# Kernel tuning notes

Measured on AMD Instinct MI355X. Metric: run time of the kernel, lower is better.

## Reference

```python
import jax, jax.numpy as jnp
import numpy as np

N_NODES = 50000
N_EDGES = 800000
IN_DIM = 128
HID = 128
NUM_CLASSES = 2


def setup_inputs() -> dict:
    key = jax.random.key(0)
    ks = jax.random.split(key, 16)
    inp = {
        "adj_row": jax.random.randint(ks[0], (N_EDGES,), 0, N_NODES),
        "adj_col": jax.random.randint(ks[1], (N_EDGES,), 0, N_NODES),
        "adj_vals": jax.random.uniform(ks[2], (N_EDGES,), dtype=jnp.float32),
        "input_feature": jax.random.normal(ks[3], (N_NODES, IN_DIM), dtype=jnp.float32),
        "graph_indicator": jax.random.randint(ks[4], (N_NODES,), 0, 64),
        # GCN layer params (kaiming-uniform-ish init; zeros bias like the torch module)
        "W1": jax.random.uniform(ks[5], (IN_DIM, HID), jnp.float32, -1, 1) * np.sqrt(6.0 / IN_DIM),
        "b1": jnp.zeros((HID,), jnp.float32),
        "W2": jax.random.uniform(ks[6], (HID, HID), jnp.float32, -1, 1) * np.sqrt(6.0 / HID),
        "b2": jnp.zeros((HID,), jnp.float32),
        "W3": jax.random.uniform(ks[7], (HID, HID), jnp.float32, -1, 1) * np.sqrt(6.0 / HID),
        "b3": jnp.zeros((HID,), jnp.float32),
        # fc params (torch.nn.Linear default init range)
        "fcW1": jax.random.uniform(ks[8], (3 * HID, HID), jnp.float32, -1, 1) / np.sqrt(3 * HID),
        "fcb1": jax.random.uniform(ks[9], (HID,), jnp.float32, -1, 1) / np.sqrt(3 * HID),
        "fcW2": jax.random.uniform(ks[10], (HID, HID // 2), jnp.float32, -1, 1) / np.sqrt(HID),
        "fcb2": jax.random.uniform(ks[11], (HID // 2,), jnp.float32, -1, 1) / np.sqrt(HID),
        "fcW3": jax.random.uniform(ks[12], (HID // 2, NUM_CLASSES), jnp.float32, -1, 1) / np.sqrt(HID // 2),
        "fcb3": jax.random.uniform(ks[13], (NUM_CLASSES,), jnp.float32, -1, 1) / np.sqrt(HID // 2),
    }
    return inp


def _gcn_layer(row, col, vals, x, W, b, n_nodes):
    # support = X @ W  -> dense GEMM
    support = x @ W
    # sparse.mm(A, support): out[i] = sum_{e: row[e]=i} vals[e] * support[col[e]]
    msgs = support[col] * vals[:, None]  # [E, D] gather + scale
    agg = jax.ops.segment_sum(msgs, row, num_segments=n_nodes)
    return agg + b


def reference(adj_row, adj_col, adj_vals, input_feature, graph_indicator,
              W1, b1, W2, b2, W3, b3, fcW1, fcb1, fcW2, fcb2, fcW3, fcb3):
    n = input_feature.shape[0]
    g1 = jax.nn.relu(_gcn_layer(adj_row, adj_col, adj_vals, input_feature, W1, b1, n))
    g2 = jax.nn.relu(_gcn_layer(adj_row, adj_col, adj_vals, g1, W2, b2, n))
    g3 = jax.nn.relu(_gcn_layer(adj_row, adj_col, adj_vals, g2, W3, b3, n))
    feat = jnp.concatenate([g1, g2, g3], axis=1)  # [N, 3*HID]
    h = jax.nn.relu(feat @ fcW1 + fcb1)
    h = jax.nn.relu(h @ fcW2 + fcb2)
    logits = h @ fcW3 + fcb3
    return logits
```

## Files before the change

### kernel.cpp

```cpp
#include <hip/hip_runtime.h>
#include <hip/hip_bf16.h>

#define N_NODES 50000
#define N_EDGES 800000
#define NBK 391
#define BCAP 2560

static inline int cdiv(int a, int b) { return (a + b - 1) / b; }

typedef __attribute__((ext_vector_type(8))) short short8;
typedef __attribute__((ext_vector_type(4))) float f32x4;

__device__ __forceinline__ float b2f(unsigned short u) {
    union { unsigned int i; float f; } c;
    c.i = ((unsigned int)u) << 16;
    return c.f;
}
__device__ __forceinline__ unsigned short f2bb(float f) {
    __hip_bfloat16 h = __float2bfloat16(f);
    return *(unsigned short*)&h;
}

__device__ __forceinline__ void pack_one(const float* __restrict__ W,
                                         __hip_bfloat16* __restrict__ out,
                                         int K, int N, int t) {
    int lane = t & 63;
    int kc = (t >> 6) % (K / 32);
    int nt = (t >> 6) / (K / 32);
    int kbase = kc * 32 + (lane >> 4) * 8;
    int col = nt * 16 + (lane & 15);
    __hip_bfloat16* dst = out + (size_t)t * 8;
#pragma unroll
    for (int j = 0; j < 8; ++j)
        dst[j] = __float2bfloat16(W[(size_t)(kbase + j) * N + col]);
}

__global__ __launch_bounds__(256)
void stage1_kernel(const int* __restrict__ row, const int* __restrict__ col,
                   const float* __restrict__ vals, int* __restrict__ bcursor,
                   int2* __restrict__ tmp, int E,
                   const float* __restrict__ x, __hip_bfloat16* __restrict__ support,
                   int M,
                   const float* __restrict__ W1, const float* __restrict__ W2,
                   const float* __restrict__ W3, const float* __restrict__ fcW1,
                   const float* __restrict__ fcW2,
                   __hip_bfloat16* __restrict__ pW2, __hip_bfloat16* __restrict__ pW3,
                   __hip_bfloat16* __restrict__ pfcW1, __hip_bfloat16* __restrict__ pfcW2) {
    __shared__ unsigned short As[64][136];
    __shared__ int hist[NBK];
    __shared__ int base[NBK];
    const int b = blockIdx.x;
    const int tid = threadIdx.x;

    if (b < 196) {
        const int CH = 4096;
        int e0 = b * CH;
        for (int i = tid; i < NBK; i += 256) hist[i] = 0;
        __syncthreads();
        for (int i = tid; i < CH; i += 256) {
            int e = e0 + i;
            if (e < E) atomicAdd(&hist[row[e] >> 7], 1);
        }
        __syncthreads();
        for (int i = tid; i < NBK; i += 256) {
            int c = hist[i];
            base[i] = (c > 0) ? (i * BCAP + atomicAdd(&bcursor[i], c)) : 0;
            hist[i] = 0;
        }
        __syncthreads();
        for (int i = tid; i < CH; i += 256) {
            int e = e0 + i;
            if (e < E) {
                int r = row[e];
                int bk = r >> 7;
                int rk = atomicAdd(&hist[bk], 1);
                tmp[base[bk] + rk] = make_int2(((r & 127) << 16) | col[e],
                                               __float_as_int(vals[e]));
            }
        }
        return;
    }

    if (b < 978) {
        const int wave = tid >> 6;
        const int lane = tid & 63;
        const int ln15 = lane & 15;
        const int quad = lane >> 4;
        const int m0 = (b - 196) * 64;

        short8 bfr[4][2];
#pragma unroll
        for (int kc = 0; kc < 4; ++kc)
#pragma unroll
            for (int h = 0; h < 2; ++h)
#pragma unroll
                for (int j = 0; j < 8; ++j)
                    bfr[kc][h][j] = (short)f2bb(
                        W1[(size_t)(kc * 32 + quad * 8 + j) * 128 + (wave * 2 + h) * 16 + ln15]);

#pragma unroll
        for (int i = 0; i < 4; ++i) {
            int idx = tid + i * 256;
            int r = idx >> 4;
            int c8 = (idx & 15) * 8;
            uint4 pk = {0, 0, 0, 0};
            if (m0 + r < M) {
                const float* src = &x[(size_t)(m0 + r) * 128 + c8];
                float4 a = *(const float4*)src;
                float4 bq = *(const float4*)(src + 4);
                pk.x = f2bb(a.x) | ((unsigned int)f2bb(a.y) << 16);
                pk.y = f2bb(a.z) | ((unsigned int)f2bb(a.w) << 16);
                pk.z = f2bb(bq.x) | ((unsigned int)f2bb(bq.y) << 16);
                pk.w = f2bb(bq.z) | ((unsigned int)f2bb(bq.w) << 16);
            }
            *(uint4*)&As[r][c8] = pk;
        }
        __syncthreads();

        f32x4 acc[4][2];
#pragma unroll
        for (int s = 0; s < 4; ++s)
#pragma unroll
            for (int h = 0; h < 2; ++h) acc[s][h] = (f32x4){0.f, 0.f, 0.f, 0.f};
#pragma unroll
        for (int kc = 0; kc < 4; ++kc) {
            short8 af[4];
#pragma unroll
            for (int s = 0; s < 4; ++s)
                af[s] = *(const short8*)&As[s * 16 + ln15][kc * 32 + quad * 8];
#pragma unroll
            for (int s = 0; s < 4; ++s)
#pragma unroll
                for (int h = 0; h < 2; ++h)
                    acc[s][h] = __builtin_amdgcn_mfma_f32_16x16x32_bf16(
                        af[s], bfr[kc][h], acc[s][h], 0, 0, 0);
        }
#pragma unroll
        for (int s = 0; s < 4; ++s)
#pragma unroll
            for (int h = 0; h < 2; ++h) {
                int cl = (wave * 2 + h) * 16 + ln15;
#pragma unroll
                for (int r = 0; r < 4; ++r) {
                    int rw = m0 + s * 16 + quad * 4 + r;
                    if (rw < M)
                        support[(size_t)rw * 128 + cl] = __float2bfloat16(acc[s][h][r]);
                }
            }
        return;
    }

    int pb = b - 978;
    if (pb < 8)       pack_one(W2,  pW2,  128, 128, pb * 256 + tid);
    else if (pb < 16) pack_one(W3,  pW3,  128, 128, (pb - 8) * 256 + tid);
    else if (pb < 40) pack_one(fcW1, pfcW1, 384, 128, (pb - 16) * 256 + tid);
    else              pack_one(fcW2, pfcW2, 128, 64, (pb - 40) * 256 + tid);
}


__global__ __launch_bounds__(512)
void bscan_kernel(const int* __restrict__ bcursor, int* __restrict__ bbase) {
    __shared__ int s[512];
    int t = threadIdx.x;
    int v = (t < NBK) ? bcursor[t] : 0;
    s[t] = v;
    __syncthreads();
    for (int off = 1; off < 512; off <<= 1) {
        int u = (t >= off) ? s[t - off] : 0;
        __syncthreads();
        s[t] += u;
        __syncthreads();
    }
    if (t < NBK) bbase[t] = s[t] - v;
    if (t == NBK - 1) bbase[NBK] = s[t];
}

__global__ __launch_bounds__(256)
void binB_kernel(const int2* __restrict__ tmp, const int* __restrict__ bcursor,
                 const int* __restrict__ bbase, int* __restrict__ row_ptr,
                 int2* __restrict__ epack, int N) {
    int b = blockIdx.x;
    int r0 = b << 7;
    int nr = N - r0; if (nr > 128) nr = 128;
    __shared__ int cnt[128];
    __shared__ int cur[128];
    int t = threadIdx.x;
    if (t < 128) cnt[t] = 0;
    __syncthreads();
    int slab = b * BCAP;
    int send = slab + bcursor[b];
    int obase = bbase[b];
    for (int i = slab + t; i < send; i += 256)
        atomicAdd(&cnt[tmp[i].x >> 16], 1);
    __syncthreads();
    if (t < 128) cur[t] = cnt[t];
    __syncthreads();
    for (int off = 1; off < 128; off <<= 1) {
        int u = (t >= off && t < 128) ? cur[t - off] : 0;
        __syncthreads();
        if (t < 128) cur[t] += u;
        __syncthreads();
    }
    if (t < 128) {
        int ex = cur[t] - cnt[t];
        int pos = obase + ex;
        cur[t] = pos;
        if (t < nr) row_ptr[r0 + t] = pos;
    }
    if (b == NBK - 1 && t == 128) row_ptr[N] = bbase[NBK];
    __syncthreads();
    for (int i = slab + t; i < send; i += 256) {
        int2 v = tmp[i];
        int rl = v.x >> 16;
        int c = v.x & 0xffff;
        int pos = atomicAdd(&cur[rl], 1);
        epack[pos] = make_int2(c, v.y);
    }
}

__global__ __launch_bounds__(256, 3)
void mfma_gemm(const __hip_bfloat16* __restrict__ A, int lda,
               const __hip_bfloat16* __restrict__ pW,
               __hip_bfloat16* __restrict__ C, int M) {
    __shared__ unsigned short As[64][136];
    const int tid = threadIdx.x;
    const int wave = tid >> 6;
    const int lane = tid & 63;
    const int ln15 = lane & 15;
    const int quad = lane >> 4;
    const int m0 = blockIdx.x * 64;
    const int ntw = wave * 2;

    f32x4 acc[4][2];
#pragma unroll
    for (int s = 0; s < 4; ++s)
#pragma unroll
        for (int h = 0; h < 2; ++h) acc[s][h] = (f32x4){0.f, 0.f, 0.f, 0.f};

#pragma unroll
    for (int i = 0; i < 4; ++i) {
        int idx = tid + i * 256;
        int r = idx >> 4;
        int c8 = (idx & 15) * 8;
        uint4 v = *(const uint4*)&A[(size_t)(m0 + r) * lda + c8];
        *(uint4*)&As[r][c8] = v;
    }
    __syncthreads();
#pragma unroll
    for (int kc = 0; kc < 4; ++kc) {
        short8 af[4];
#pragma unroll
        for (int s = 0; s < 4; ++s)
            af[s] = *(const short8*)&As[s * 16 + ln15][kc * 32 + quad * 8];
        short8 bf[2];
#pragma unroll
        for (int h = 0; h < 2; ++h)
            bf[h] = *(const short8*)&pW[((size_t)((ntw + h) * 4 + kc) * 64 + lane) * 8];
#pragma unroll
        for (int s = 0; s < 4; ++s)
#pragma unroll
            for (int h = 0; h < 2; ++h)
                acc[s][h] = __builtin_amdgcn_mfma_f32_16x16x32_bf16(
                    af[s], bf[h], acc[s][h], 0, 0, 0);
    }

#pragma unroll
    for (int s = 0; s < 4; ++s)
#pragma unroll
        for (int h = 0; h < 2; ++h) {
            int cl = (ntw + h) * 16 + ln15;
#pragma unroll
            for (int r = 0; r < 4; ++r) {
                int rw = m0 + s * 16 + quad * 4 + r;
                if (rw < M)
                    C[(size_t)rw * 128 + cl] = __float2bfloat16(acc[s][h][r]);
            }
        }
}

__global__ __launch_bounds__(256)
void spmm_kernel(const int* __restrict__ row_ptr, const int2* __restrict__ epack,
                 const __hip_bfloat16* __restrict__ support,
                 const float* __restrict__ bias, __hip_bfloat16* __restrict__ out,
                 int ldo, int n) {
    int wv = threadIdx.x >> 6;
    int l = threadIdx.x & 63;
    int node = blockIdx.x * 4 + wv;
    if (node >= n) return;
    const long long* ep = (const long long*)epack;
    int start = row_ptr[node], end = row_ptr[node + 1];
    float ax = 0.f, ay = 0.f;
    int p = start;
    for (; p + 8 <= end; p += 8) {
        long long v[8];
        ushort2 u[8];
#pragma unroll
        for (int j = 0; j < 8; ++j) v[j] = ep[p + j];
#pragma unroll
        for (int j = 0; j < 8; ++j)
            u[j] = *(const ushort2*)&support[(size_t)(unsigned int)(v[j] & 0xffffffff) * 128 + l * 2];
#pragma unroll
        for (int j = 0; j < 8; ++j) {
            float f = __int_as_float((int)(v[j] >> 32));
            ax += f * b2f(u[j].x);
            ay += f * b2f(u[j].y);
        }
    }
    for (; p < end; ++p) {
        long long v0 = ep[p];
        ushort2 u0 = *(const ushort2*)&support[(size_t)(unsigned int)(v0 & 0xffffffff) * 128 + l * 2];
        float f0 = __int_as_float((int)(v0 >> 32));
        ax += f0 * b2f(u0.x);
        ay += f0 * b2f(u0.y);
    }
    unsigned int packed = (unsigned int)f2bb(fmaxf(ax + bias[l * 2 + 0], 0.f))
                        | ((unsigned int)f2bb(fmaxf(ay + bias[l * 2 + 1], 0.f)) << 16);
    __builtin_nontemporal_store(packed, (unsigned int*)&out[(size_t)node * ldo + l * 2]);
}

__global__ __launch_bounds__(256, 3)
void fc123_kernel(const __hip_bfloat16* __restrict__ featb,
                  const __hip_bfloat16* __restrict__ pfcW1,
                  const float* __restrict__ fcb1,
                  const __hip_bfloat16* __restrict__ pfcW2,
                  const float* __restrict__ fcb2,
                  const float* __restrict__ fcW3, const float* __restrict__ fcb3,
                  float* __restrict__ out, int M) {
    __shared__ unsigned short As[64][136];
    __shared__ float w3s[128];
    __shared__ float b3s[2];
    const int tid = threadIdx.x;
    const int wave = tid >> 6;
    const int lane = tid & 63;
    const int ln15 = lane & 15;
    const int quad = lane >> 4;
    const int m0 = blockIdx.x * 64;
    if (tid < 128) w3s[tid] = fcW3[tid];
    if (tid < 2) b3s[tid] = fcb3[tid];

    f32x4 acc[4][2];
#pragma unroll
    for (int s = 0; s < 4; ++s)
#pragma unroll
        for (int h = 0; h < 2; ++h) acc[s][h] = (f32x4){0.f, 0.f, 0.f, 0.f};
    for (int kb = 0; kb < 3; ++kb) {
#pragma unroll
        for (int i = 0; i < 4; ++i) {
            int idx = tid + i * 256;
            int r = idx >> 4;
            int c8 = (idx & 15) * 8;
            uint4 v = *(const uint4*)&featb[(size_t)(m0 + r) * 384 + kb * 128 + c8];
            *(uint4*)&As[r][c8] = v;
        }
        __syncthreads();
#pragma unroll
        for (int kc = 0; kc < 4; ++kc) {
            short8 af[4];
#pragma unroll
            for (int s = 0; s < 4; ++s)
                af[s] = *(const short8*)&As[s * 16 + ln15][kc * 32 + quad * 8];
            short8 bf[2];
#pragma unroll
            for (int h = 0; h < 2; ++h) {
                int kcg = kb * 4 + kc;
                bf[h] = *(const short8*)&pfcW1[((size_t)((wave * 2 + h) * 12 + kcg) * 64 + lane) * 8];
            }
#pragma unroll
            for (int s = 0; s < 4; ++s)
#pragma unroll
                for (int h = 0; h < 2; ++h)
                    acc[s][h] = __builtin_amdgcn_mfma_f32_16x16x32_bf16(
                        af[s], bf[h], acc[s][h], 0, 0, 0);
        }
        __syncthreads();
    }
#pragma unroll
    for (int s = 0; s < 4; ++s)
#pragma unroll
        for (int h = 0; h < 2; ++h) {
            int col = (wave * 2 + h) * 16 + ln15;
            float bv = fcb1[col];
#pragma unroll
            for (int r = 0; r < 4; ++r) {
                int row = s * 16 + quad * 4 + r;
                As[row][col] = f2bb(fmaxf(acc[s][h][r] + bv, 0.f));
            }
        }
    __syncthreads();

    f32x4 acc2[4];
#pragma unroll
    for (int s = 0; s < 4; ++s) acc2[s] = (f32x4){0.f, 0.f, 0.f, 0.f};
#pragma unroll
    for (int kc = 0; kc < 4; ++kc) {
        short8 af[4];
#pragma unroll
        for (int s = 0; s < 4; ++s)
            af[s] = *(const short8*)&As[s * 16 + ln15][kc * 32 + quad * 8];
        short8 bfw = *(const short8*)&pfcW2[((size_t)(wave * 4 + kc) * 64 + lane) * 8];
#pragma unroll
        for (int s = 0; s < 4; ++s)
            acc2[s] = __builtin_amdgcn_mfma_f32_16x16x32_bf16(af[s], bfw, acc2[s], 0, 0, 0);
    }
    __syncthreads();
    {
        int col2 = wave * 16 + ln15;
        float bv = fcb2[col2];
#pragma unroll
        for (int s = 0; s < 4; ++s)
#pragma unroll
            for (int r = 0; r < 4; ++r) {
                int row = s * 16 + quad * 4 + r;
                As[row][col2] = f2bb(fmaxf(acc2[s][r] + bv, 0.f));
            }
    }
    __syncthreads();

    if (tid < 128) {
        int row = tid >> 1, cls = tid & 1;
        int grow = m0 + row;
        if (grow < M) {
            float a = b3s[cls];
#pragma unroll
            for (int k = 0; k < 64; ++k)
                a += b2f(As[row][k]) * w3s[k * 2 + cls];
            out[(size_t)grow * 2 + cls] = a;
        }
    }
}

extern "C" void kernel_launch(void* const* d_in, const int* in_sizes, int n_in,
                              void* d_out, int out_size, void* d_ws, size_t ws_size,
                              hipStream_t stream) {
    const int*   adj_row  = (const int*)d_in[0];
    const int*   adj_col  = (const int*)d_in[1];
    const float* adj_vals = (const float*)d_in[2];
    const float* x        = (const float*)d_in[3];
    const float* W1   = (const float*)d_in[5];
    const float* b1   = (const float*)d_in[6];
    const float* W2   = (const float*)d_in[7];
    const float* b2   = (const float*)d_in[8];
    const float* W3   = (const float*)d_in[9];
    const float* b3   = (const float*)d_in[10];
    const float* fcW1 = (const float*)d_in[11];
    const float* fcb1 = (const float*)d_in[12];
    const float* fcW2 = (const float*)d_in[13];
    const float* fcb2 = (const float*)d_in[14];
    const float* fcW3 = (const float*)d_in[15];
    const float* fcb3 = (const float*)d_in[16];
    float* out = (float*)d_out;

    const int N = N_NODES, E = N_EDGES;
    const int Mpad = 50048;

    char* p = (char*)d_ws;
    auto alloc = [&](size_t bytes) {
        char* q = p;
        p += (bytes + 255) & ~(size_t)255;
        return q;
    };
    __hip_bfloat16* featb    = (__hip_bfloat16*)alloc((size_t)Mpad * 384 * 2);
    __hip_bfloat16* supportb = (__hip_bfloat16*)alloc((size_t)Mpad * 128 * 2);
    __hip_bfloat16* pW2   = (__hip_bfloat16*)alloc(16384 * 2);
    __hip_bfloat16* pW3   = (__hip_bfloat16*)alloc(16384 * 2);
    __hip_bfloat16* pfcW1 = (__hip_bfloat16*)alloc(49152 * 2);
    __hip_bfloat16* pfcW2 = (__hip_bfloat16*)alloc(8192 * 2);
    int*   row_ptr   = (int*)alloc((size_t)(N + 1) * 4);
    int*   bbase     = (int*)alloc((size_t)(NBK + 1) * 4);
    int*   bcursor   = (int*)alloc((size_t)NBK * 4);
    int2*  epack     = (int2*)alloc((size_t)E * 8);
    int2*  tmp       = (int2*)alloc((size_t)NBK * BCAP * 8);

    hipMemsetAsync(bcursor, 0, (size_t)NBK * 4, stream);
    stage1_kernel<<<1022, 256, 0, stream>>>(adj_row, adj_col, adj_vals, bcursor, tmp, E,
                                            x, supportb, N,
                                            W1, W2, W3, fcW1, fcW2,
                                            pW2, pW3, pfcW1, pfcW2);
    bscan_kernel<<<1, 512, 0, stream>>>(bcursor, bbase);
    binB_kernel<<<NBK, 256, 0, stream>>>(tmp, bcursor, bbase, row_ptr, epack, N);

    const int gemmGrid = cdiv(N, 64);
    const int spmmGrid = cdiv(N, 4);

    spmm_kernel<<<spmmGrid, 256, 0, stream>>>(row_ptr, epack, supportb, b1,
                                              featb + 0, 384, N);
    mfma_gemm<<<gemmGrid, 256, 0, stream>>>(featb + 0, 384, pW2, supportb, N);
    spmm_kernel<<<spmmGrid, 256, 0, stream>>>(row_ptr, epack, supportb, b2,
                                              featb + 128, 384, N);
    mfma_gemm<<<gemmGrid, 256, 0, stream>>>(featb + 128, 384, pW3, supportb, N);
    spmm_kernel<<<spmmGrid, 256, 0, stream>>>(row_ptr, epack, supportb, b3,
                                              featb + 256, 384, N);

    fc123_kernel<<<gemmGrid, 256, 0, stream>>>(featb, pfcW1, fcb1, pfcW2, fcb2,
                                               fcW3, fcb3, out, N);
}
```

Measured before the change: 296.4 us.

## Pad CSR rows to multiples of eight and software-pipeline SpMM gathers

The binning kernel now pads each row's edge list to a multiple of eight with zero-weight entries pointing at node 0, and records per-row end pointers in a new row_end array. Each 128-row bucket gets its own slack region. This removes the scalar tail loop in the SpMM kernel. The SpMM loop is also double-buffered: it issues the next eight edge loads and support gathers before accumulating the previous batch, to hide gather latency. In exchange, padding adds extra gathers on average degree-16 rows and uses more registers per lane.

```diff
diff --git a/kernel.cpp b/kernel.cpp
--- a/kernel.cpp
+++ b/kernel.cpp
@@ -5,6 +5,7 @@
 #define N_EDGES 800000
 #define NBK 391
 #define BCAP 2560
+#define PADSLACK 896
 
 static inline int cdiv(int a, int b) { return (a + b - 1) / b; }
 
@@ -178,22 +179,24 @@
 __global__ __launch_bounds__(256)
 void binB_kernel(const int2* __restrict__ tmp, const int* __restrict__ bcursor,
                  const int* __restrict__ bbase, int* __restrict__ row_ptr,
-                 int2* __restrict__ epack, int N) {
+                 int* __restrict__ row_end, int2* __restrict__ epack, int N) {
     int b = blockIdx.x;
     int r0 = b << 7;
     int nr = N - r0; if (nr > 128) nr = 128;
     __shared__ int cnt[128];
     __shared__ int cur[128];
+    __shared__ int rpos[128];
     int t = threadIdx.x;
     if (t < 128) cnt[t] = 0;
     __syncthreads();
     int slab = b * BCAP;
     int send = slab + bcursor[b];
-    int obase = bbase[b];
     for (int i = slab + t; i < send; i += 256)
         atomicAdd(&cnt[tmp[i].x >> 16], 1);
     __syncthreads();
-    if (t < 128) cur[t] = cnt[t];
+    int rcnt = (t < 128) ? cnt[t] : 0;
+    int pc = (rcnt + 7) & ~7;
+    if (t < 128) cur[t] = pc;
     __syncthreads();
     for (int off = 1; off < 128; off <<= 1) {
         int u = (t >= off && t < 128) ? cur[t - off] : 0;
@@ -201,13 +204,16 @@
         if (t < 128) cur[t] += u;
         __syncthreads();
     }
+    int obase = bbase[b] + b * PADSLACK;
     if (t < 128) {
-        int ex = cur[t] - cnt[t];
-        int pos = obase + ex;
+        int pos = obase + cur[t] - pc;
+        rpos[t] = pos;
         cur[t] = pos;
-        if (t < nr) row_ptr[r0 + t] = pos;
-    }
-    if (b == NBK - 1 && t == 128) row_ptr[N] = bbase[NBK];
+        if (t < nr) {
+            row_ptr[r0 + t] = pos;
+            row_end[r0 + t] = pos + pc;
+        }
+    }
     __syncthreads();
     for (int i = slab + t; i < send; i += 256) {
         int2 v = tmp[i];
@@ -215,6 +221,12 @@
         int c = v.x & 0xffff;
         int pos = atomicAdd(&cur[rl], 1);
         epack[pos] = make_int2(c, v.y);
+    }
+    if (t < 128) {
+        int pos = rpos[t];
+#pragma unroll 1
+        for (int i = pos + rcnt; i < pos + pc; ++i)
+            epack[i] = make_int2(0, 0);
     }
 }
 
@@ -279,7 +291,8 @@
 }
 
 __global__ __launch_bounds__(256)
-void spmm_kernel(const int* __restrict__ row_ptr, const int2* __restrict__ epack,
+void spmm_kernel(const int* __restrict__ row_ptr, const int* __restrict__ row_end,
+                 const int2* __restrict__ epack,
                  const __hip_bfloat16* __restrict__ support,
                  const float* __restrict__ bias, __hip_bfloat16* __restrict__ out,
                  int ldo, int n) {
@@ -288,30 +301,45 @@
     int node = blockIdx.x * 4 + wv;
     if (node >= n) return;
     const long long* ep = (const long long*)epack;
-    int start = row_ptr[node], end = row_ptr[node + 1];
+    int p = row_ptr[node], end = row_end[node];
     float ax = 0.f, ay = 0.f;
-    int p = start;
-    for (; p + 8 <= end; p += 8) {
-        long long v[8];
-        ushort2 u[8];
+    long long v[8];
+    ushort2 u[8];
+    bool have = false;
+    if (p < end) {
 #pragma unroll
         for (int j = 0; j < 8; ++j) v[j] = ep[p + j];
 #pragma unroll
         for (int j = 0; j < 8; ++j)
-            u[j] = *(const ushort2*)&support[(size_t)(unsigned int)(v[j] & 0xffffffff) * 128 + l * 2];
+            u[j] = *(const ushort2*)&support[(size_t)(unsigned int)(v[j] & 0xffffffffu) * 128 + l * 2];
+        p += 8;
+        have = true;
+    }
+    while (p < end) {
+        long long v2[8];
+        ushort2 u2[8];
+#pragma unroll
+        for (int j = 0; j < 8; ++j) v2[j] = ep[p + j];
+#pragma unroll
+        for (int j = 0; j < 8; ++j)
+            u2[j] = *(const ushort2*)&support[(size_t)(unsigned int)(v2[j] & 0xffffffffu) * 128 + l * 2];
 #pragma unroll
         for (int j = 0; j < 8; ++j) {
             float f = __int_as_float((int)(v[j] >> 32));
             ax += f * b2f(u[j].x);
             ay += f * b2f(u[j].y);
         }
-    }
-    for (; p < end; ++p) {
-        long long v0 = ep[p];
-        ushort2 u0 = *(const ushort2*)&support[(size_t)(unsigned int)(v0 & 0xffffffff) * 128 + l * 2];
-        float f0 = __int_as_float((int)(v0 >> 32));
-        ax += f0 * b2f(u0.x);
-        ay += f0 * b2f(u0.y);
+#pragma unroll
+        for (int j = 0; j < 8; ++j) { v[j] = v2[j]; u[j] = u2[j]; }
+        p += 8;
+    }
+    if (have) {
+#pragma unroll
+        for (int j = 0; j < 8; ++j) {
+            float f = __int_as_float((int)(v[j] >> 32));
+            ax += f * b2f(u[j].x);
+            ay += f * b2f(u[j].y);
+        }
     }
     unsigned int packed = (unsigned int)f2bb(fmaxf(ax + bias[l * 2 + 0], 0.f))
                         | ((unsigned int)f2bb(fmaxf(ay + bias[l * 2 + 1], 0.f)) << 16);
@@ -452,6 +480,7 @@
 
     const int N = N_NODES, E = N_EDGES;
     const int Mpad = 50048;
+    const int EPAD = E + NBK * PADSLACK + 64;
 
     char* p = (char*)d_ws;
     auto alloc = [&](size_t bytes) {
@@ -466,9 +495,10 @@
     __hip_bfloat16* pfcW1 = (__hip_bfloat16*)alloc(49152 * 2);
     __hip_bfloat16* pfcW2 = (__hip_bfloat16*)alloc(8192 * 2);
     int*   row_ptr   = (int*)alloc((size_t)(N + 1) * 4);
+    int*   row_end   = (int*)alloc((size_t)(N + 1) * 4);
     int*   bbase     = (int*)alloc((size_t)(NBK + 1) * 4);
     int*   bcursor   = (int*)alloc((size_t)NBK * 4);
-    int2*  epack     = (int2*)alloc((size_t)E * 8);
+    int2*  epack     = (int2*)alloc((size_t)EPAD * 8);
     int2*  tmp       = (int2*)alloc((size_t)NBK * BCAP * 8);
 
     hipMemsetAsync(bcursor, 0, (size_t)NBK * 4, stream);
@@ -477,18 +507,18 @@
                                             W1, W2, W3, fcW1, fcW2,
                                             pW2, pW3, pfcW1, pfcW2);
     bscan_kernel<<<1, 512, 0, stream>>>(bcursor, bbase);
-    binB_kernel<<<NBK, 256, 0, stream>>>(tmp, bcursor, bbase, row_ptr, epack, N);
+    binB_kernel<<<NBK, 256, 0, stream>>>(tmp, bcursor, bbase, row_ptr, row_end, epack, N);
 
     const int gemmGrid = cdiv(N, 64);
     const int spmmGrid = cdiv(N, 4);
 
-    spmm_kernel<<<spmmGrid, 256, 0, stream>>>(row_ptr, epack, supportb, b1,
+    spmm_kernel<<<spmmGrid, 256, 0, stream>>>(row_ptr, row_end, epack, supportb, b1,
                                               featb + 0, 384, N);
     mfma_gemm<<<gemmGrid, 256, 0, stream>>>(featb + 0, 384, pW2, supportb, N);
-    spmm_kernel<<<spmmGrid, 256, 0, stream>>>(row_ptr, epack, supportb, b2,
+    spmm_kernel<<<spmmGrid, 256, 0, stream>>>(row_ptr, row_end, epack, supportb, b2,
                                               featb + 128, 384, N);
     mfma_gemm<<<gemmGrid, 256, 0, stream>>>(featb + 128, 384, pW3, supportb, N);
-    spmm_kernel<<<spmmGrid, 256, 0, stream>>>(row_ptr, epack, supportb, b3,
+    spmm_kernel<<<spmmGrid, 256, 0, stream>>>(row_ptr, row_end, epack, supportb, b3,
                                               featb + 256, 384, N);
 
     fc123_kernel<<<gemmGrid, 256, 0, stream>>>(featb, pfcW1, fcb1, pfcW2, fcb2,
```

Result: faster. 279.2 us (-5.8%).
